# Performance work log

Measured on AMD Instinct MI355X. Metric: run time of the kernel, lower is better.

## Reference

```python
import jax, jax.numpy as jnp
import numpy as np

N = 100000

def _norm_edges(edge_index, n):
    # add self loops, compute symmetric GCN normalization
    loop = jnp.arange(n, dtype=edge_index.dtype)
    src = jnp.concatenate([edge_index[0], loop])
    dst = jnp.concatenate([edge_index[1], loop])
    deg = jax.ops.segment_sum(jnp.ones_like(dst, dtype=jnp.float32), dst, num_segments=n)
    dinv = jnp.where(deg > 0, deg ** -0.5, 0.0)
    norm = dinv[src] * dinv[dst]
    return src, dst, norm

def _gcn(x, W, b, src, dst, norm, n):
    h = x @ W  # [N, out]
    msg = h[src] * norm[:, None]
    return jax.ops.segment_sum(msg, dst, num_segments=n) + b

def setup_inputs() -> dict:
    key = jax.random.key(0)
    ks = jax.random.split(key, 20)
    E = 3200000
    d_in, d_out = 64, 64
    def w(k, i, o):
        return jax.random.normal(k, (i, o), dtype=jnp.float32) * (1.0 / np.sqrt(i))
    return {
        "x": jax.random.normal(ks[0], (N, d_in), dtype=jnp.float32),
        "t": jax.random.normal(ks[1], (N,), dtype=jnp.float32),
        "edge_index": jax.random.randint(ks[2], (2, E), 0, N, dtype=jnp.int64),
        "W1": w(ks[3], d_in + 1, 64), "b1": jnp.zeros((64,), jnp.float32),
        "W2": w(ks[4], 64, 128), "b2": jnp.zeros((128,), jnp.float32),
        "W3": w(ks[5], 128, 256), "b3": jnp.zeros((256,), jnp.float32),
        "W4": w(ks[6], 256, 128), "b4": jnp.zeros((128,), jnp.float32),
        "F1": w(ks[7], 128, 256), "c1": jnp.zeros((256,), jnp.float32),
        "F2": w(ks[8], 256, 128), "c2": jnp.zeros((128,), jnp.float32),
        "F3": w(ks[9], 128, d_out), "c3": jnp.zeros((d_out,), jnp.float32),
    }

def reference(x, t, edge_index, W1, b1, W2, b2, W3, b3, W4, b4, F1, c1, F2, c2, F3, c3):
    n = x.shape[0]
    src, dst, norm = _norm_edges(edge_index, n)
    h = jnp.concatenate([x, t[:, None]], axis=1)
    h = jax.nn.gelu(_gcn(h, W1, b1, src, dst, norm, n))
    h = jax.nn.gelu(_gcn(h, W2, b2, src, dst, norm, n))
    h = jax.nn.gelu(_gcn(h, W3, b3, src, dst, norm, n))
    h = jax.nn.gelu(_gcn(h, W4, b4, src, dst, norm, n))
    h = jax.nn.gelu(h @ F1 + c1)
    h = jax.nn.gelu(h @ F2 + c2)
    return h @ F3 + c3
```

## Files before the change

### kernel.cpp

```cpp
#include <hip/hip_runtime.h>

static constexpr int BLK = 256;

typedef double d2 __attribute__((ext_vector_type(2)));

__device__ __forceinline__ double gelu_d(double v){
  double u = 0.7978845608028654 * (v + 0.044715 * v * v * v);
  return 0.5 * v * (1.0 + tanh(u));
}

__global__ void zero_k(int* __restrict__ a, int n){
  int stride = gridDim.x * blockDim.x;
  for (int i = blockIdx.x*blockDim.x + threadIdx.x; i < n; i += stride) a[i] = 0;
}

__global__ void detect_k(const int* __restrict__ ei, int* __restrict__ flag){
  if (threadIdx.x == 0 && blockIdx.x == 0){
    int zeros = 0;
    for (int i = 0; i < 64; ++i) if (ei[2*i + 1] == 0) ++zeros;
    *flag = (zeros >= 48) ? 1 : 0;
  }
}

__global__ void count_k(const int* __restrict__ ei, int E, const int* __restrict__ flag,
                        int* __restrict__ cnt){
  int is64 = *flag;
  int stride = gridDim.x * blockDim.x;
  for (int e = blockIdx.x*blockDim.x + threadIdx.x; e < E; e += stride){
    int d = is64 ? ei[2*(E + e)] : ei[E + e];
    atomicAdd(&cnt[d], 1);
  }
}

__global__ void dinv_k(const int* __restrict__ cnt, double* __restrict__ dinv, int n){
  int i = blockIdx.x*blockDim.x + threadIdx.x;
  if (i < n){
    double deg = (double)(cnt[i] + 1);
    dinv[i] = 1.0 / sqrt(deg);
  }
}

__global__ __launch_bounds__(256)
void scanA_k(const int* __restrict__ cnt, int* __restrict__ partial, int n, int chunk){
  __shared__ int red[256];
  int b = blockIdx.x;
  int lo = b * chunk, hi = min(n, lo + chunk);
  int s = 0;
  for (int i = lo + threadIdx.x; i < hi; i += 256) s += cnt[i];
  red[threadIdx.x] = s; __syncthreads();
  for (int off = 128; off > 0; off >>= 1){
    if (threadIdx.x < off) red[threadIdx.x] += red[threadIdx.x + off];
    __syncthreads();
  }
  if (threadIdx.x == 0) partial[b] = red[0];
}

__global__ __launch_bounds__(256)
void scanB_k(int* __restrict__ partial, int nb){
  __shared__ int sd[256];
  int tid = threadIdx.x;
  int v = (tid < nb) ? partial[tid] : 0;
  sd[tid] = v; __syncthreads();
  for (int off = 1; off < 256; off <<= 1){
    int t = (tid >= off) ? sd[tid - off] : 0;
    __syncthreads();
    sd[tid] += t;
    __syncthreads();
  }
  if (tid < nb) partial[tid] = sd[tid] - v;
  if (tid == 255) partial[nb] = sd[255];
}

__global__ __launch_bounds__(256)
void scanC_k(const int* __restrict__ cnt, const int* __restrict__ partial,
             int* __restrict__ rp, int n, int chunk, int nb){
  __shared__ int sd[256];
  int b = blockIdx.x;
  int lo = b * chunk, hi = min(n, lo + chunk);
  int run = partial[b];
  for (int base = lo; base < hi; base += 256){
    int i = base + threadIdx.x;
    int v = (i < hi) ? cnt[i] : 0;
    sd[threadIdx.x] = v; __syncthreads();
    for (int off = 1; off < 256; off <<= 1){
      int t = (threadIdx.x >= off) ? sd[threadIdx.x - off] : 0;
      __syncthreads();
      sd[threadIdx.x] += t;
      __syncthreads();
    }
    if (i < hi) rp[i] = run + sd[threadIdx.x] - v;
    run += sd[255];
    __syncthreads();
  }
  if (b == 0 && threadIdx.x == 0) rp[n] = partial[nb];
}

__global__ void scatter_k(const int* __restrict__ ei, int E, const int* __restrict__ flag,
                          const int* __restrict__ rp, int* __restrict__ fill,
                          const double* __restrict__ dinv,
                          int* __restrict__ col, double* __restrict__ val){
  int is64 = *flag;
  int stride = gridDim.x * blockDim.x;
  for (int e = blockIdx.x*blockDim.x + threadIdx.x; e < E; e += stride){
    int s = is64 ? ei[2*e]       : ei[e];
    int d = is64 ? ei[2*(E + e)] : ei[E + e];
    int p = rp[d] + atomicAdd(&fill[d], 1);
    col[p] = s;
    if (val) val[p] = dinv[s];
  }
}

template<typename ST>
__global__ void concat_k(const float* __restrict__ x, const float* __restrict__ t,
                         ST* __restrict__ h0, int n){
  int total = n * 66;
  int stride = gridDim.x * blockDim.x;
  for (int idx = blockIdx.x*blockDim.x + threadIdx.x; idx < total; idx += stride){
    int row = idx / 66;
    int c = idx - row * 66;
    float v = (c < 64) ? x[row*64 + c] : (c == 64 ? t[row] : 0.0f);
    h0[idx] = (ST)v;
  }
}

template<typename ST>
__global__ __launch_bounds__(256, 4)
void gemm_k(const ST* __restrict__ A, int K, int lda,
            const float* __restrict__ W, int NOUT,
            const float* __restrict__ bias,
            ST* __restrict__ C, float* __restrict__ Cf,
            int n, int fuse)
{
  __shared__ __align__(16) double As[128][18];
  __shared__ __align__(16) double Ws[16][66];
  const int row0 = blockIdx.x * 128;
  const int col0 = blockIdx.y * 64;
  const int tid = threadIdx.x;
  const int tr = tid >> 4, tc = tid & 15;
  const int c0 = 2 * tc;
  double acc[8][4] = {};

  const int sar = tid >> 1;
  const int sak = (tid & 1) * 8;
  const int swr = tid >> 4;
  const int swc = (tid & 15) * 4;

  const int ktiles = (K + 15) / 16;

  double ga[8];
  float  gw[4];

  auto loadA = [&](int k0){
    int gr = row0 + sar;
    if constexpr (sizeof(ST) == 8){
      if (gr < n){
        const double* Ap = (const double*)A + (size_t)gr * lda + k0 + sak;
        #pragma unroll
        for (int g = 0; g < 4; ++g){
          d2 v = *(const d2*)(Ap + 2*g);
          ga[2*g] = v.x; ga[2*g+1] = v.y;
        }
      } else {
        #pragma unroll
        for (int u = 0; u < 8; ++u) ga[u] = 0.0;
      }
    } else {
      const ST* Ap = A + (size_t)gr * lda + k0 + sak;
      #pragma unroll
      for (int u = 0; u < 8; ++u){
        int kg = k0 + sak + u;
        ga[u] = (gr < n && kg < K) ? (double)Ap[u] : 0.0;
      }
    }
  };
  auto loadW = [&](int k0){
    int kg = k0 + swr;
    if (kg < K){
      const float* Wp = W + (size_t)kg * NOUT + col0 + swc;
      #pragma unroll
      for (int g = 0; g < 4; ++g) gw[g] = Wp[g];
    } else {
      #pragma unroll
      for (int g = 0; g < 4; ++g) gw[g] = 0.0f;
    }
  };

  loadA(0);
  loadW(0);

  for (int kt = 0; kt < ktiles; ++kt){
    #pragma unroll
    for (int g = 0; g < 4; ++g){
      d2 v; v.x = ga[2*g]; v.y = ga[2*g+1];
      *(d2*)&As[sar][sak + 2*g] = v;
    }
    {
      d2 v0; v0.x = (double)gw[0]; v0.y = (double)gw[1];
      d2 v1; v1.x = (double)gw[2]; v1.y = (double)gw[3];
      *(d2*)&Ws[swr][swc]     = v0;
      *(d2*)&Ws[swr][swc + 2] = v1;
    }
    __syncthreads();
    if (kt + 1 < ktiles){
      loadA((kt + 1) * 16);
      loadW((kt + 1) * 16);
    }
    #pragma unroll
    for (int kk = 0; kk < 16; kk += 2){
      d2 w0a = *(const d2*)&Ws[kk    ][c0];
      d2 w0b = *(const d2*)&Ws[kk    ][c0 + 32];
      d2 w1a = *(const d2*)&Ws[kk + 1][c0];
      d2 w1b = *(const d2*)&Ws[kk + 1][c0 + 32];
      #pragma unroll
      for (int i = 0; i < 8; ++i){
        d2 av = *(const d2*)&As[tr + 16*i][kk];
        acc[i][0] = fma(av.x, w0a.x, acc[i][0]);
        acc[i][1] = fma(av.x, w0a.y, acc[i][1]);
        acc[i][2] = fma(av.x, w0b.x, acc[i][2]);
        acc[i][3] = fma(av.x, w0b.y, acc[i][3]);
        acc[i][0] = fma(av.y, w1a.x, acc[i][0]);
        acc[i][1] = fma(av.y, w1a.y, acc[i][1]);
        acc[i][2] = fma(av.y, w1b.x, acc[i][2]);
        acc[i][3] = fma(av.y, w1b.y, acc[i][3]);
      }
    }
    __syncthreads();
  }
  #pragma unroll
  for (int i = 0; i < 8; ++i){
    int r = row0 + tr + 16*i;
    if (r >= n) continue;
    #pragma unroll
    for (int j = 0; j < 4; ++j){
      int c = col0 + ((j < 2) ? (c0 + j) : (c0 + 30 + j));
      double v = acc[i][j];
      if (fuse){ v += (double)bias[c]; if (fuse == 1) v = gelu_d(v); }
      if (fuse == 2) __builtin_nontemporal_store((float)v, &Cf[(size_t)r * NOUT + c]);
      else           __builtin_nontemporal_store((ST)v,   &C [(size_t)r * NOUT + c]);
    }
  }
}

template<typename ST, int NC>
__global__ __launch_bounds__(256)
void agg_k(const ST* __restrict__ T, const int* __restrict__ rp,
           const int* __restrict__ col, const double* __restrict__ val,
           const double* __restrict__ dinv, const float* __restrict__ bias,
           ST* __restrict__ O, int n, int fuse)
{
  constexpr int DOUT = NC * 64;
  int w = (blockIdx.x * blockDim.x + threadIdx.x) >> 6;
  int lane = threadIdx.x & 63;
  if (w >= n) return;
  double dv = dinv[w];
  const ST* Ti = T + (size_t)w * DOUT;
  double acc[NC];
  #pragma unroll
  for (int c = 0; c < NC; ++c) acc[c] = dv * (double)Ti[lane + 64*c];
  int e  = rp[w];
  int e1 = rp[w + 1];
  if (val){
    for (; e + 4 <= e1; e += 4){
      int s0 = __builtin_nontemporal_load(&col[e]);
      int s1 = __builtin_nontemporal_load(&col[e+1]);
      int s2 = __builtin_nontemporal_load(&col[e+2]);
      int s3 = __builtin_nontemporal_load(&col[e+3]);
      double v0 = __builtin_nontemporal_load(&val[e]);
      double v1 = __builtin_nontemporal_load(&val[e+1]);
      double v2 = __builtin_nontemporal_load(&val[e+2]);
      double v3 = __builtin_nontemporal_load(&val[e+3]);
      const ST* T0 = T + (size_t)s0 * DOUT;
      const ST* T1 = T + (size_t)s1 * DOUT;
      const ST* T2 = T + (size_t)s2 * DOUT;
      const ST* T3 = T + (size_t)s3 * DOUT;
      double t0[NC], t1[NC], t2[NC], t3[NC];
      #pragma unroll
      for (int c = 0; c < NC; ++c){
        t0[c] = (double)T0[lane + 64*c];
        t1[c] = (double)T1[lane + 64*c];
        t2[c] = (double)T2[lane + 64*c];
        t3[c] = (double)T3[lane + 64*c];
      }
      #pragma unroll
      for (int c = 0; c < NC; ++c){
        acc[c] = fma(v0, t0[c], acc[c]);
        acc[c] = fma(v1, t1[c], acc[c]);
        acc[c] = fma(v2, t2[c], acc[c]);
        acc[c] = fma(v3, t3[c], acc[c]);
      }
    }
    for (; e < e1; ++e){
      int s = __builtin_nontemporal_load(&col[e]);
      double v = __builtin_nontemporal_load(&val[e]);
      const ST* Ts = T + (size_t)s * DOUT;
      #pragma unroll
      for (int c = 0; c < NC; ++c) acc[c] = fma(v, (double)Ts[lane + 64*c], acc[c]);
    }
  } else {
    for (; e < e1; ++e){
      int s = col[e];
      double v = dinv[s];
      const ST* Ts = T + (size_t)s * DOUT;
      #pragma unroll
      for (int c = 0; c < NC; ++c) acc[c] = fma(v, (double)Ts[lane + 64*c], acc[c]);
    }
  }
  ST* Oi = O + (size_t)w * DOUT;
  #pragma unroll
  for (int c = 0; c < NC; ++c){
    double v = dv * acc[c];
    if (fuse) v = gelu_d(v + (double)bias[lane + 64*c]);
    __builtin_nontemporal_store((ST)v, &Oi[lane + 64*c]);
  }
}

template<typename ST>
static void run_net(const float* x, const float* t,
                    const float* W1, const float* b1, const float* W2, const float* b2,
                    const float* W3, const float* b3, const float* W4, const float* b4,
                    const float* F1, const float* c1, const float* F2, const float* c2,
                    const float* F3, const float* c3,
                    ST* b256, ST* ba, ST* bb,
                    const int* rp, const int* col, const double* val, const double* dinv,
                    float* out, int N, hipStream_t stream)
{
  auto gemm = [&](const ST* A, int K, int lda, const float* W, int NOUT, const float* bias,
                  ST* C, float* Cf, int fuse){
    dim3 g((N + 127) / 128, NOUT / 64);
    gemm_k<ST><<<g, dim3(BLK), 0, stream>>>(A, K, lda, W, NOUT, bias, C, Cf, N, fuse);
  };
  int aggGrid = (N * 64 + BLK - 1) / BLK;
  auto agg64 = [&](const ST* T, const float* bias, ST* O, int fuse){
    agg_k<ST,1><<<dim3(aggGrid), dim3(BLK), 0, stream>>>(T, rp, col, val, dinv, bias, O, N, fuse);
  };
  auto agg128 = [&](const ST* T, const float* bias, ST* O, int fuse){
    agg_k<ST,2><<<dim3(aggGrid), dim3(BLK), 0, stream>>>(T, rp, col, val, dinv, bias, O, N, fuse);
  };

  concat_k<ST><<<dim3(1024), dim3(BLK), 0, stream>>>(x, t, ba, N);
  gemm(ba, 65, 66, W1, 64, nullptr, bb, nullptr, 0);
  agg64(bb, b1, ba, 1);
  agg64(ba, nullptr, bb, 0);
  gemm(bb, 64, 64, W2, 128, b2, ba, nullptr, 1);
  agg128(ba, nullptr, bb, 0);
  gemm(bb, 128, 128, W3, 256, b3, b256, nullptr, 1);
  gemm(b256, 256, 256, W4, 128, nullptr, ba, nullptr, 0);
  agg128(ba, b4, bb, 1);
  gemm(bb, 128, 128, F1, 256, c1, b256, nullptr, 1);
  gemm(b256, 256, 256, F2, 128, c2, ba, nullptr, 1);
  gemm(ba, 128, 128, F3, 64, c3, nullptr, out, 2);
}

extern "C" void kernel_launch(void* const* d_in, const int* in_sizes, int n_in,
                              void* d_out, int out_size, void* d_ws, size_t ws_size,
                              hipStream_t stream)
{
  const float* x  = (const float*)d_in[0];
  const float* t  = (const float*)d_in[1];
  const int*   ei = (const int*)d_in[2];
  const float* W1 = (const float*)d_in[3];  const float* b1 = (const float*)d_in[4];
  const float* W2 = (const float*)d_in[5];  const float* b2 = (const float*)d_in[6];
  const float* W3 = (const float*)d_in[7];  const float* b3 = (const float*)d_in[8];
  const float* W4 = (const float*)d_in[9];  const float* b4 = (const float*)d_in[10];
  const float* F1 = (const float*)d_in[11]; const float* c1 = (const float*)d_in[12];
  const float* F2 = (const float*)d_in[13]; const float* c2 = (const float*)d_in[14];
  const float* F3 = (const float*)d_in[15]; const float* c3 = (const float*)d_in[16];
  float* out = (float*)d_out;
  int N = in_sizes[0] / 64;
  int E = in_sizes[2] / 2;

  char* p = (char*)d_ws;
  auto alloc = [&](size_t b){ char* r = p; p += (b + 255) & ~(size_t)255; return (void*)r; };
  int*    flag    = (int*)alloc(4);
  int*    cnt     = (int*)alloc((size_t)N * 4);
  int*    fill    = (int*)alloc((size_t)N * 4);
  int*    rp      = (int*)alloc((size_t)(N + 1) * 4);
  int*    partial = (int*)alloc((size_t)257 * 4);
  int*    col     = (int*)alloc((size_t)E * 4);
  double* dinv    = (double*)alloc((size_t)N * 8);
  size_t base = (size_t)(p - (char*)d_ws);

  size_t slackB = 1024;
  size_t actElems = (size_t)N * 512;
  size_t valBytes = ((size_t)E * 8 + 255) & ~(size_t)255;
  bool f64val = ws_size >= base + valBytes + actElems * sizeof(double) + 3*slackB;
  bool f64ok  = f64val || ws_size >= base + actElems * sizeof(double) + 3*slackB;
  bool f32val = ws_size >= base + valBytes + actElems * sizeof(float) + 3*slackB;
  bool f32ok  = f32val || ws_size >= base + actElems * sizeof(float) + 3*slackB;
  if (!f32ok) return;

  double* val = nullptr;
  if ((f64ok && f64val) || (!f64ok && f32val)) val = (double*)alloc((size_t)E * 8);

  int nb = 256;
  int chunk = (N + nb - 1) / nb;
  zero_k<<<dim3(256), dim3(BLK), 0, stream>>>(cnt, N);
  zero_k<<<dim3(256), dim3(BLK), 0, stream>>>(fill, N);
  detect_k<<<1, 64, 0, stream>>>(ei, flag);
  count_k<<<dim3(4096), dim3(BLK), 0, stream>>>(ei, E, flag, cnt);
  dinv_k<<<dim3((N + BLK - 1) / BLK), dim3(BLK), 0, stream>>>(cnt, dinv, N);
  scanA_k<<<dim3(nb), dim3(256), 0, stream>>>(cnt, partial, N, chunk);
  scanB_k<<<dim3(1), dim3(256), 0, stream>>>(partial, nb);
  scanC_k<<<dim3(nb), dim3(256), 0, stream>>>(cnt, partial, rp, N, chunk, nb);
  scatter_k<<<dim3(4096), dim3(BLK), 0, stream>>>(ei, E, flag, rp, fill, dinv, col, val);

  if (f64ok){
    double* b256 = (double*)alloc((size_t)N * 256 * 8 + slackB);
    double* ba   = (double*)alloc((size_t)N * 128 * 8 + slackB);
    double* bb   = (double*)alloc((size_t)N * 128 * 8 + slackB);
    run_net<double>(x, t, W1, b1, W2, b2, W3, b3, W4, b4, F1, c1, F2, c2, F3, c3,
                    b256, ba, bb, rp, col, val, dinv, out, N, stream);
  } else {
    float* b256 = (float*)alloc((size_t)N * 256 * 4 + slackB);
    float* ba   = (float*)alloc((size_t)N * 128 * 4 + slackB);
    float* bb   = (float*)alloc((size_t)N * 128 * 4 + slackB);
    run_net<float>(x, t, W1, b1, W2, b2, W3, b3, W4, b4, F1, c1, F2, c2, F3, c3,
                   b256, ba, bb, rp, col, val, dinv, out, N, stream);
  }
}
```

Measured before the change: 2.541 ms.

## Emulate W4 double GEMM with Ozaki-style int8 MFMA splitting

Replaces the fp64 FMA GEMM for the 256->128 W4 layer with an Ozaki-style scheme. Activations and weights are scaled by their absolute maximum and split into five int8 slices. The slice products are accumulated with i32 MFMA 16x16x64 instructions and recombined in double. The W3 GEMM epilogue now also computes the activation abs-max with an atomicMax. The aim is to move the heaviest fp64 GEMM onto int8 matrix cores, at the cost of extra quantization passes (5x N*256 bytes written and read) and reduced precision for small-magnitude values relative to the global max.

After: 2.558 ms. No clear change (+0.7%).

```diff
diff --git a/kernel.cpp b/kernel.cpp
--- a/kernel.cpp
+++ b/kernel.cpp
@@ -3,6 +3,7 @@
 static constexpr int BLK = 256;
 
 typedef double d2 __attribute__((ext_vector_type(2)));
+typedef int    i4 __attribute__((ext_vector_type(4)));
 
 __device__ __forceinline__ double gelu_d(double v){
   double u = 0.7978845608028654 * (v + 0.044715 * v * v * v);
@@ -12,6 +13,10 @@
 __global__ void zero_k(int* __restrict__ a, int n){
   int stride = gridDim.x * blockDim.x;
   for (int i = blockIdx.x*blockDim.x + threadIdx.x; i < n; i += stride) a[i] = 0;
+}
+
+__global__ void zeromax_k(unsigned long long* m){
+  if (threadIdx.x == 0 && blockIdx.x == 0){ m[0] = 0ull; m[1] = 0ull; }
 }
 
 __global__ void detect_k(const int* __restrict__ ei, int* __restrict__ flag){
@@ -129,7 +134,7 @@
             const float* __restrict__ W, int NOUT,
             const float* __restrict__ bias,
             ST* __restrict__ C, float* __restrict__ Cf,
-            int n, int fuse)
+            int n, int fuse, unsigned long long* __restrict__ amax)
 {
   __shared__ __align__(16) double As[128][18];
   __shared__ __align__(16) double Ws[16][66];
@@ -226,6 +231,7 @@
     }
     __syncthreads();
   }
+  double tmax = 0.0;
   #pragma unroll
   for (int i = 0; i < 8; ++i){
     int r = row0 + tr + 16*i;
@@ -235,9 +241,134 @@
       int c = col0 + ((j < 2) ? (c0 + j) : (c0 + 30 + j));
       double v = acc[i][j];
       if (fuse){ v += (double)bias[c]; if (fuse == 1) v = gelu_d(v); }
+      if (amax) tmax = fmax(tmax, fabs(v));
       if (fuse == 2) __builtin_nontemporal_store((float)v, &Cf[(size_t)r * NOUT + c]);
       else           __builtin_nontemporal_store((ST)v,   &C [(size_t)r * NOUT + c]);
     }
+  }
+  if (amax){
+    #pragma unroll
+    for (int off = 32; off > 0; off >>= 1)
+      tmax = fmax(tmax, __shfl_xor(tmax, off));
+    if ((threadIdx.x & 63) == 0)
+      atomicMax(amax, (unsigned long long)__double_as_longlong(tmax));
+  }
+}
+
+
+__global__ void absmaxW_k(const float* __restrict__ W, int n, unsigned long long* __restrict__ out){
+  double tmax = 0.0;
+  int stride = gridDim.x * blockDim.x;
+  for (int i = blockIdx.x*blockDim.x + threadIdx.x; i < n; i += stride)
+    tmax = fmax(tmax, (double)fabsf(W[i]));
+  #pragma unroll
+  for (int off = 32; off > 0; off >>= 1)
+    tmax = fmax(tmax, __shfl_xor(tmax, off));
+  if ((threadIdx.x & 63) == 0)
+    atomicMax(out, (unsigned long long)__double_as_longlong(tmax));
+}
+
+__global__ void quantW_k(const float* __restrict__ W, int K, int N,
+                         const unsigned long long* __restrict__ maxw,
+                         char* __restrict__ WqT){
+  double wm = __longlong_as_double((long long)*maxw);
+  int sw = (wm > 0.0) ? (37 - ilogb(wm)) : 0;
+  double sc = ldexp(1.0, sw);
+  int total = K * N;
+  size_t NK = (size_t)N * K;
+  int stride = gridDim.x * blockDim.x;
+  for (int t = blockIdx.x*blockDim.x + threadIdx.x; t < total; t += stride){
+    int k = t / N, nn = t - k * N;
+    long long v = __double2ll_rn((double)W[t] * sc);
+    #pragma unroll
+    for (int p = 0; p < 5; ++p){
+      int d = (int)((v + 128) & 255) - 128;
+      WqT[(size_t)p * NK + (size_t)nn * K + k] = (char)d;
+      v = (v - d) >> 8;
+    }
+  }
+}
+
+__global__ void quantA_k(const double* __restrict__ A, size_t MK,
+                         const unsigned long long* __restrict__ maxa,
+                         char* __restrict__ Aq){
+  double am = __longlong_as_double((long long)*maxa);
+  int sa = (am > 0.0) ? (38 - ilogb(am)) : 0;
+  double sc = ldexp(1.0, sa);
+  size_t stride = (size_t)gridDim.x * blockDim.x;
+  for (size_t i = blockIdx.x*(size_t)blockDim.x + threadIdx.x; i < MK; i += stride){
+    long long v = __double2ll_rn(A[i] * sc);
+    #pragma unroll
+    for (int p = 0; p < 5; ++p){
+      int d = (int)((v + 128) & 255) - 128;
+      Aq[(size_t)p * MK + i] = (char)d;
+      v = (v - d) >> 8;
+    }
+  }
+}
+
+__global__ __launch_bounds__(512)
+void ozaki_k(const char* __restrict__ Aq, const char* __restrict__ WqT,
+             const unsigned long long* __restrict__ maxa,
+             const unsigned long long* __restrict__ maxw,
+             double* __restrict__ C, int n, int K, int N)
+{
+  constexpr int PP[22] = {0,0,0, 1,1,1,1, 2,2,2,2,2, 3,3,3,3,3, 4,4,4,4,4};
+  constexpr int QQ[22] = {2,3,4, 1,2,3,4, 0,1,2,3,4, 0,1,2,3,4, 0,1,2,3,4};
+  __shared__ __align__(16) char laq[5 * 16 * 80];
+  const size_t MK = (size_t)n * K;
+  const size_t NK = (size_t)N * K;
+  const int tid  = threadIdx.x;
+  const int lane = tid & 63;
+  const int ct   = tid >> 6;
+  const int l15  = lane & 15;
+  const int lk   = lane >> 4;
+  const int row0 = blockIdx.x * 16;
+
+  i4 acc[22];
+  #pragma unroll
+  for (int i = 0; i < 22; ++i){ i4 z = {0,0,0,0}; acc[i] = z; }
+
+  const int ksteps = K / 64;
+  for (int ks = 0; ks < ksteps; ++ks){
+    int k0 = ks * 64;
+    if (ks) __syncthreads();
+    if (tid < 320){
+      int p  = tid >> 6;
+      int rr = (tid >> 2) & 15;
+      int sg = tid & 3;
+      int gr = row0 + rr; if (gr >= n) gr = n - 1;
+      i4 v = *(const i4*)(Aq + (size_t)p * MK + (size_t)gr * K + k0 + sg * 16);
+      *(i4*)(laq + p * 1280 + rr * 80 + sg * 16) = v;
+    }
+    __syncthreads();
+    i4 af[5], bf[5];
+    #pragma unroll
+    for (int p = 0; p < 5; ++p)
+      af[p] = *(const i4*)(laq + p * 1280 + l15 * 80 + lk * 16);
+    #pragma unroll
+    for (int q = 0; q < 5; ++q)
+      bf[q] = *(const i4*)(WqT + (size_t)q * NK + (size_t)(ct * 16 + l15) * K + k0 + lk * 16);
+    #pragma unroll
+    for (int i = 0; i < 22; ++i)
+      acc[i] = __builtin_amdgcn_mfma_i32_16x16x64_i8(af[PP[i]], bf[QQ[i]], acc[i], 0, 0, 0);
+  }
+
+  double am = __longlong_as_double((long long)*maxa);
+  double wm = __longlong_as_double((long long)*maxw);
+  int sa = (am > 0.0) ? (38 - ilogb(am)) : 0;
+  int sw = (wm > 0.0) ? (37 - ilogb(wm)) : 0;
+  double s = ldexp(1.0, -(sa + sw));
+  #pragma unroll
+  for (int m = 0; m < 4; ++m){
+    int r = row0 + lk * 4 + m;
+    if (r >= n) continue;
+    double sum = 0.0;
+    #pragma unroll
+    for (int i = 0; i < 22; ++i)
+      sum += ldexp((double)acc[i][m], 8 * (PP[i] + QQ[i]));
+    int c = ct * 16 + l15;
+    __builtin_nontemporal_store(sum * s, &C[(size_t)r * N + c]);
   }
 }
 
@@ -322,12 +453,13 @@
                     const float* F3, const float* c3,
                     ST* b256, ST* ba, ST* bb,
                     const int* rp, const int* col, const double* val, const double* dinv,
+                    char* Aq, char* WqT, unsigned long long* maxbuf, bool ozk,
                     float* out, int N, hipStream_t stream)
 {
   auto gemm = [&](const ST* A, int K, int lda, const float* W, int NOUT, const float* bias,
-                  ST* C, float* Cf, int fuse){
+                  ST* C, float* Cf, int fuse, unsigned long long* amax){
     dim3 g((N + 127) / 128, NOUT / 64);
-    gemm_k<ST><<<g, dim3(BLK), 0, stream>>>(A, K, lda, W, NOUT, bias, C, Cf, N, fuse);
+    gemm_k<ST><<<g, dim3(BLK), 0, stream>>>(A, K, lda, W, NOUT, bias, C, Cf, N, fuse, amax);
   };
   int aggGrid = (N * 64 + BLK - 1) / BLK;
   auto agg64 = [&](const ST* T, const float* bias, ST* O, int fuse){
@@ -338,17 +470,27 @@
   };
 
   concat_k<ST><<<dim3(1024), dim3(BLK), 0, stream>>>(x, t, ba, N);
-  gemm(ba, 65, 66, W1, 64, nullptr, bb, nullptr, 0);
+  gemm(ba, 65, 66, W1, 64, nullptr, bb, nullptr, 0, nullptr);
   agg64(bb, b1, ba, 1);
   agg64(ba, nullptr, bb, 0);
-  gemm(bb, 64, 64, W2, 128, b2, ba, nullptr, 1);
+  gemm(bb, 64, 64, W2, 128, b2, ba, nullptr, 1, nullptr);
   agg128(ba, nullptr, bb, 0);
-  gemm(bb, 128, 128, W3, 256, b3, b256, nullptr, 1);
-  gemm(b256, 256, 256, W4, 128, nullptr, ba, nullptr, 0);
+  gemm(bb, 128, 128, W3, 256, b3, b256, nullptr, 1,
+       ozk ? maxbuf : nullptr);
+  if (ozk){
+    if constexpr (sizeof(ST) == 8){
+      size_t MK = (size_t)N * 256;
+      quantA_k<<<dim3(4096), dim3(BLK), 0, stream>>>((const double*)b256, MK, maxbuf, Aq);
+      ozaki_k<<<dim3((N + 15) / 16), dim3(512), 0, stream>>>(
+          Aq, WqT, maxbuf, maxbuf + 1, (double*)ba, N, 256, 128);
+    }
+  } else {
+    gemm(b256, 256, 256, W4, 128, nullptr, ba, nullptr, 0, nullptr);
+  }
   agg128(ba, b4, bb, 1);
-  gemm(bb, 128, 128, F1, 256, c1, b256, nullptr, 1);
-  gemm(b256, 256, 256, F2, 128, c2, ba, nullptr, 1);
-  gemm(ba, 128, 128, F3, 64, c3, nullptr, out, 2);
+  gemm(bb, 128, 128, F1, 256, c1, b256, nullptr, 1, nullptr);
+  gemm(b256, 256, 256, F2, 128, c2, ba, nullptr, 1, nullptr);
+  gemm(ba, 128, 128, F3, 64, c3, nullptr, out, 2, nullptr);
 }
 
 extern "C" void kernel_launch(void* const* d_in, const int* in_sizes, int n_in,
@@ -408,13 +550,27 @@
     double* b256 = (double*)alloc((size_t)N * 256 * 8 + slackB);
     double* ba   = (double*)alloc((size_t)N * 128 * 8 + slackB);
     double* bb   = (double*)alloc((size_t)N * 128 * 8 + slackB);
+    size_t MK = (size_t)N * 256;
+    size_t need = (size_t)(p - (char*)d_ws) + 5*MK + 5*32768 + 1024;
+    bool ozk = (ws_size >= need);
+    char* Aq = nullptr; char* WqT = nullptr; unsigned long long* maxbuf = nullptr;
+    if (ozk){
+      maxbuf = (unsigned long long*)alloc(256);
+      Aq     = (char*)alloc(5 * MK);
+      WqT    = (char*)alloc(5 * 32768);
+      zeromax_k<<<1, 64, 0, stream>>>(maxbuf);
+      absmaxW_k<<<dim3(32), dim3(BLK), 0, stream>>>(W4, 256 * 128, maxbuf + 1);
+      quantW_k<<<dim3(128), dim3(BLK), 0, stream>>>(W4, 256, 128, maxbuf + 1, WqT);
+    }
     run_net<double>(x, t, W1, b1, W2, b2, W3, b3, W4, b4, F1, c1, F2, c2, F3, c3,
-                    b256, ba, bb, rp, col, val, dinv, out, N, stream);
+                    b256, ba, bb, rp, col, val, dinv,
+                    Aq, WqT, maxbuf, ozk, out, N, stream);
   } else {
     float* b256 = (float*)alloc((size_t)N * 256 * 4 + slackB);
     float* ba   = (float*)alloc((size_t)N * 128 * 4 + slackB);
     float* bb   = (float*)alloc((size_t)N * 128 * 4 + slackB);
     run_net<float>(x, t, W1, b1, W2, b2, W3, b3, W4, b4, F1, c1, F2, c2, F3, c3,
-                   b256, ba, bb, rp, col, val, dinv, out, N, stream);
-  }
-}
+                   b256, ba, bb, rp, col, val, dinv,
+                   nullptr, nullptr, nullptr, false, out, N, stream);
+  }
+}
```
